# Optimization experiments

Measured on AMD Instinct MI355X. Metric: run time of the kernel, lower is better.

The kernel has to match this reference:

```python
import jax, jax.numpy as jnp
import numpy as np

B, D3, DQ, H, UNITS, SK = 32, 1024, 1024, 1024, 1024, 1024


def setup_inputs() -> dict:
    key = jax.random.key(0)
    ks = jax.random.split(key, 11)
    return {
        "K": jax.random.normal(ks[0], (B, SK, UNITS), jnp.float32),
        "Q": jax.random.normal(ks[1], (B, DQ, D3), jnp.float32),
        "M": jax.random.normal(ks[2], (B, D3, D3), jnp.float32),
        "ht": jax.random.normal(ks[3], (B, D3, H), jnp.float32),
        "Wp": jax.random.normal(ks[4], (D3, DQ), jnp.float32) * 0.02,
        "bp": jax.random.normal(ks[5], (D3,), jnp.float32) * 0.02,
        "W3": jax.random.normal(ks[6], (D3, D3), jnp.float32) * 0.02,
        "W4": jax.random.normal(ks[7], (D3, D3), jnp.float32) * 0.02,
        "b3": jax.random.normal(ks[8], (D3,), jnp.float32) * 0.02,
        "Wd": jax.random.normal(ks[9], (H + D3, UNITS), jnp.float32) * 0.02,
        "bd": jax.random.normal(ks[10], (UNITS,), jnp.float32) * 0.02,
    }


def reference(K, Q, M, ht, Wp, bp, W3, W4, b3, Wd, bd):
    # q = Wp @ Q + bp  -> (B, d3, d3); bp broadcasts over the last axis
    q = jnp.einsum('ij,bjk->bik', Wp, Q) + bp
    # concat([ht, q], axis=-1) -> (B, d3, h + d3), then fresh Dense(units)
    concat = jnp.concatenate([ht, q], axis=-1)
    mlp = jnp.einsum('bdc,cu->bdu', concat, Wd) + bd  # (B, d3, units)
    # scores = K @ mlp^T, softmax over last axis (computed but unused in the
    # original layer's output -- kept for faithfulness; DCE'd under jit)
    scores = jnp.einsum('bsu,bdu->bsd', K, mlp)       # (B, sK, d3)
    distribution = jax.nn.softmax(scores, axis=-1)
    del distribution
    # Belta = relu(W3 @ M + W4 @ q + b3), gated multiply with q
    Belta = jax.nn.relu(
        jnp.einsum('ij,bjk->bik', W3, M)
        + jnp.einsum('ij,bjk->bik', W4, q)
        + b3
    )
    q_new = Belta * q  # (B, d3, d3)
    return q_new
```

## Files before the change

### kernel.cpp

```cpp
#include <hip/hip_runtime.h>
#include <hip/hip_bf16.h>
#include <stdint.h>


#define D_ 1024

typedef __attribute__((ext_vector_type(8))) short short8;
typedef __attribute__((ext_vector_type(4))) float floatx4;
typedef __attribute__((ext_vector_type(4))) unsigned short us4;

__device__ __forceinline__ unsigned short f2bf(float f) {
  union { float f; unsigned int u; } v; v.f = f;
  unsigned int u = v.u;
  unsigned int r = (u + 0x7FFFu + ((u >> 16) & 1u)) >> 16;
  return (unsigned short)r;
}

__device__ __forceinline__ float bf2f(unsigned short h) {
  union { unsigned int u; float f; } v; v.u = ((unsigned int)h) << 16;
  return v.f;
}

__device__ __forceinline__ void async_load16(const void* g, void* l) {
  __builtin_amdgcn_global_load_lds(
      (const __attribute__((address_space(1))) unsigned int*)g,
      (__attribute__((address_space(3))) unsigned int*)l, 16, 0, 0);
}

__global__ __launch_bounds__(256) void transpose_cvt(
    const float* __restrict__ in, unsigned short* __restrict__ out) {
  __shared__ float tile[64][65];
  const int b = blockIdx.z;
  const long base = ((long)b) << 20;
  const int r0 = blockIdx.y * 64, c0 = blockIdx.x * 64;
  const int t = threadIdx.x;
  const int tr = t >> 4, tc4 = (t & 15) * 4;
#pragma unroll
  for (int p = 0; p < 4; ++p) {
    const int row = p * 16 + tr;
    const float4 v = *(const float4*)&in[base + (long)(r0 + row) * D_ + c0 + tc4];
    tile[row][tc4 + 0] = v.x; tile[row][tc4 + 1] = v.y;
    tile[row][tc4 + 2] = v.z; tile[row][tc4 + 3] = v.w;
  }
  __syncthreads();
#pragma unroll
  for (int p = 0; p < 4; ++p) {
    const int c = p * 16 + tr;
    us4 pk;
    pk.x = f2bf(tile[tc4 + 0][c]);
    pk.y = f2bf(tile[tc4 + 1][c]);
    pk.z = f2bf(tile[tc4 + 2][c]);
    pk.w = f2bf(tile[tc4 + 3][c]);
    *(us4*)&out[base + (long)(c0 + c) * D_ + r0 + tc4] = pk;
  }
}

__global__ __launch_bounds__(256) void convert_weights(
    const float* __restrict__ Wp, const float* __restrict__ W3,
    const float* __restrict__ W4, unsigned short* __restrict__ Wpb,
    unsigned short* __restrict__ A2) {
  const int i = blockIdx.x * 256 + threadIdx.x;
  const long e = (long)i * 4;
  const int row = (int)(e >> 10);
  const int col = (int)(e & 1023);
  const float4 a = ((const float4*)Wp)[i];
  us4 pa; pa.x = f2bf(a.x); pa.y = f2bf(a.y); pa.z = f2bf(a.z); pa.w = f2bf(a.w);
  ((us4*)Wpb)[i] = pa;
  const float4 w3 = ((const float4*)W3)[i];
  us4 p3; p3.x = f2bf(w3.x); p3.y = f2bf(w3.y); p3.z = f2bf(w3.z); p3.w = f2bf(w3.w);
  *(us4*)&A2[(long)row * 2048 + col] = p3;
  const float4 w4 = ((const float4*)W4)[i];
  us4 p4; p4.x = f2bf(w4.x); p4.y = f2bf(w4.y); p4.z = f2bf(w4.z); p4.w = f2bf(w4.w);
  *(us4*)&A2[(long)row * 2048 + 1024 + col] = p4;
}

__global__ __launch_bounds__(256) void gemm1(
    const unsigned short* __restrict__ Wpb,
    const unsigned short* __restrict__ Qt,
    const float* __restrict__ bp,
    unsigned short* __restrict__ qt) {
  __shared__ __align__(16) unsigned short As[128 * 64];
  __shared__ __align__(16) unsigned short Bs[128 * 64];
  const int lane = threadIdx.x & 63;
  const int wave = threadIdx.x >> 6;
  const int b = blockIdx.z;
  const int m0 = blockIdx.y * 128, n0 = blockIdx.x * 128;
  const long bb = ((long)b) << 20;
  const int wm = (wave >> 1) * 64, wn = (wave & 1) * 64;

  const int srow = wave * 32 + (lane >> 3);
  const int scol = (lane & 7) * 8;

  const unsigned short* ag = Wpb + (long)(m0 + srow) * D_ + scol;
  const unsigned short* bg = Qt + bb + (long)(n0 + srow) * D_ + scol;

  floatx4 acc[4][4] = {};

  for (int kk = 0; kk < D_; kk += 64) {
    if (kk) __syncthreads();
#pragma unroll
    for (int t = 0; t < 4; ++t) {
      async_load16(ag + (long)t * 8 * D_ + kk, &As[(wave * 32 + t * 8) * 64]);
      async_load16(bg + (long)t * 8 * D_ + kk, &Bs[(wave * 32 + t * 8) * 64]);
    }
    __syncthreads();
#pragma unroll
    for (int k2 = 0; k2 < 64; k2 += 32) {
      const int krd = k2 + (lane >> 4) * 8;
      short8 af[4], bf[4];
#pragma unroll
      for (int mt = 0; mt < 4; ++mt)
        af[mt] = *(const short8*)&As[(wm + mt * 16 + (lane & 15)) * 64 + krd];
#pragma unroll
      for (int nt = 0; nt < 4; ++nt)
        bf[nt] = *(const short8*)&Bs[(wn + nt * 16 + (lane & 15)) * 64 + krd];
#pragma unroll
      for (int mt = 0; mt < 4; ++mt)
#pragma unroll
        for (int nt = 0; nt < 4; ++nt)
          acc[mt][nt] = __builtin_amdgcn_mfma_f32_16x16x32_bf16(
              af[mt], bf[nt], acc[mt][nt], 0, 0, 0);
    }
  }

  const int quad = lane >> 4;
#pragma unroll
  for (int nt = 0; nt < 4; ++nt) {
    const int col = n0 + wn + nt * 16 + (lane & 15);
    const float bias = bp[col];
#pragma unroll
    for (int mt = 0; mt < 4; ++mt) {
      const int row = m0 + wm + mt * 16 + quad * 4;
      const floatx4 v = acc[mt][nt];
      us4 pk;
      pk.x = f2bf(v.x + bias); pk.y = f2bf(v.y + bias);
      pk.z = f2bf(v.z + bias); pk.w = f2bf(v.w + bias);
      *(us4*)&qt[bb + (long)col * D_ + row] = pk;
    }
  }
}

__global__ __launch_bounds__(256) void gemm2(
    const unsigned short* __restrict__ A2,
    const unsigned short* __restrict__ Mt,
    const unsigned short* __restrict__ qt,
    const float* __restrict__ b3,
    float* __restrict__ out) {
  __shared__ __align__(16) unsigned short As[128 * 64];
  __shared__ __align__(16) unsigned short Bs[128 * 64];
  const int lane = threadIdx.x & 63;
  const int wave = threadIdx.x >> 6;
  const int b = blockIdx.z;
  const int m0 = blockIdx.y * 128, n0 = blockIdx.x * 128;
  const long bb = ((long)b) << 20;
  const int wm = (wave >> 1) * 64, wn = (wave & 1) * 64;

  const int srow = wave * 32 + (lane >> 3);
  const int scol = (lane & 7) * 8;

  const unsigned short* ag = A2 + (long)(m0 + srow) * 2048 + scol;
  const unsigned short* bg1 = Mt + bb + (long)(n0 + srow) * D_ + scol;
  const unsigned short* bg2 = qt + bb + (long)(n0 + srow) * D_ + scol;

  floatx4 acc[4][4] = {};

  for (int kk = 0; kk < 2048; kk += 64) {
    if (kk) __syncthreads();
    const unsigned short* bg = (kk < 1024) ? (bg1 + kk) : (bg2 + (kk - 1024));
#pragma unroll
    for (int t = 0; t < 4; ++t) {
      async_load16(ag + (long)t * 8 * 2048 + kk, &As[(wave * 32 + t * 8) * 64]);
      async_load16(bg + (long)t * 8 * D_, &Bs[(wave * 32 + t * 8) * 64]);
    }
    __syncthreads();
#pragma unroll
    for (int k2 = 0; k2 < 64; k2 += 32) {
      const int krd = k2 + (lane >> 4) * 8;
      short8 af[4], bf[4];
#pragma unroll
      for (int mt = 0; mt < 4; ++mt)
        af[mt] = *(const short8*)&As[(wm + mt * 16 + (lane & 15)) * 64 + krd];
#pragma unroll
      for (int nt = 0; nt < 4; ++nt)
        bf[nt] = *(const short8*)&Bs[(wn + nt * 16 + (lane & 15)) * 64 + krd];
#pragma unroll
      for (int mt = 0; mt < 4; ++mt)
#pragma unroll
        for (int nt = 0; nt < 4; ++nt)
          acc[mt][nt] = __builtin_amdgcn_mfma_f32_16x16x32_bf16(
              af[mt], bf[nt], acc[mt][nt], 0, 0, 0);
    }
  }

  const int quad = lane >> 4;
#pragma unroll
  for (int nt = 0; nt < 4; ++nt) {
    const int col = n0 + wn + nt * 16 + (lane & 15);
    const float b3v = b3[col];
#pragma unroll
    for (int mt = 0; mt < 4; ++mt) {
      const int row = m0 + wm + mt * 16 + quad * 4;
      const floatx4 v = acc[mt][nt];
      const us4 qv = *(const us4*)&qt[bb + (long)col * D_ + row];
      float t0 = fmaxf(v.x + b3v, 0.0f);
      float t1 = fmaxf(v.y + b3v, 0.0f);
      float t2 = fmaxf(v.z + b3v, 0.0f);
      float t3 = fmaxf(v.w + b3v, 0.0f);
      out[bb + (long)(row + 0) * D_ + col] = t0 * bf2f(qv.x);
      out[bb + (long)(row + 1) * D_ + col] = t1 * bf2f(qv.y);
      out[bb + (long)(row + 2) * D_ + col] = t2 * bf2f(qv.z);
      out[bb + (long)(row + 3) * D_ + col] = t3 * bf2f(qv.w);
    }
  }
}

extern "C" void kernel_launch(void* const* d_in, const int* in_sizes, int n_in,
                              void* d_out, int out_size, void* d_ws, size_t ws_size,
                              hipStream_t stream) {
  const float* Q  = (const float*)d_in[1];
  const float* M  = (const float*)d_in[2];
  const float* Wp = (const float*)d_in[4];
  const float* bp = (const float*)d_in[5];
  const float* W3 = (const float*)d_in[6];
  const float* W4 = (const float*)d_in[7];
  const float* b3 = (const float*)d_in[8];
  float* out = (float*)d_out;

  char* ws = (char*)d_ws;
  unsigned short* qt  = (unsigned short*)(ws);
  unsigned short* Qt  = (unsigned short*)(ws + (64l  << 20));
  unsigned short* Mt  = (unsigned short*)(ws + (128l << 20));
  unsigned short* Wpb = (unsigned short*)(ws + (192l << 20));
  unsigned short* A2  = (unsigned short*)(ws + (194l << 20));

  dim3 tgrid(16, 16, 32);
  transpose_cvt<<<tgrid, 256, 0, stream>>>(Q, Qt);
  transpose_cvt<<<tgrid, 256, 0, stream>>>(M, Mt);
  convert_weights<<<1024, 256, 0, stream>>>(Wp, W3, W4, Wpb, A2);

  dim3 ggrid(8, 8, 32);
  gemm1<<<ggrid, 256, 0, stream>>>(Wpb, Qt, bp, qt);
  gemm2<<<ggrid, 256, 0, stream>>>(A2, Mt, qt, b3, out);
}
```

Baseline: 759.4 us.

## Replace GEMMs with 256x256 double-buffered 8-wave ping-pong MFMA kernel

Replaces the two 128x128 single-buffered GEMM kernels with one templated 256x256-tile kernel using 8 waves, double-buffered LDS, XOR-swizzled LDS layout, and phased MFMA blocks interleaved with async global-to-LDS loads and s_setprio. The block index is swizzled so neighbouring blocks share batches and tiles. The aim is to hide load latency behind compute, cut LDS bank conflicts and raise data reuse per tile. In exchange the kernel uses 128 KB of LDS and many accumulator registers, and it relies on explicit waitcnt and barrier placement being correct.

```diff
diff --git a/kernel.cpp b/kernel.cpp
--- a/kernel.cpp
+++ b/kernel.cpp
@@ -1,5 +1,4 @@
 #include <hip/hip_runtime.h>
-#include <hip/hip_bf16.h>
 #include <stdint.h>
 
 
@@ -8,6 +7,9 @@
 typedef __attribute__((ext_vector_type(8))) short short8;
 typedef __attribute__((ext_vector_type(4))) float floatx4;
 typedef __attribute__((ext_vector_type(4))) unsigned short us4;
+
+#define VMCNT0() asm volatile("s_waitcnt vmcnt(0)" ::: "memory")
+#define LGKM0()  asm volatile("s_waitcnt lgkmcnt(0)" ::: "memory")
 
 __device__ __forceinline__ unsigned short f2bf(float f) {
   union { float f; unsigned int u; } v; v.f = f;
@@ -74,142 +76,195 @@
   *(us4*)&A2[(long)row * 2048 + 1024 + col] = p4;
 }
 
-__global__ __launch_bounds__(256) void gemm1(
-    const unsigned short* __restrict__ Wpb,
-    const unsigned short* __restrict__ Qt,
-    const float* __restrict__ bp,
-    unsigned short* __restrict__ qt) {
-  __shared__ __align__(16) unsigned short As[128 * 64];
-  __shared__ __align__(16) unsigned short Bs[128 * 64];
+template <int NT, int LDA, bool IS_G2>
+__global__ __launch_bounds__(512, 2) void gemm8p(
+    const unsigned short* __restrict__ A,
+    const unsigned short* __restrict__ B1,
+    const unsigned short* __restrict__ B2,
+    const float* __restrict__ bias,
+    void* __restrict__ outp) {
+  __shared__ __align__(16) unsigned short As[2][256 * 64];
+  __shared__ __align__(16) unsigned short Bs[2][256 * 64];
+
   const int lane = threadIdx.x & 63;
-  const int wave = threadIdx.x >> 6;
-  const int b = blockIdx.z;
-  const int m0 = blockIdx.y * 128, n0 = blockIdx.x * 128;
+  const int w = threadIdx.x >> 6;
+  const int wm = (w >> 2) * 128;
+  const int wn = (w & 3) * 64;
+  const int l15 = lane & 15;
+  const int quad = lane >> 4;
+
+  const int bid = blockIdx.x;
+  const int swz = (bid & 7) * 64 + (bid >> 3);
+  const int b = swz >> 4;
+  const int m0 = ((swz >> 2) & 3) * 256;
+  const int n0 = (swz & 3) * 256;
   const long bb = ((long)b) << 20;
-  const int wm = (wave >> 1) * 64, wn = (wave & 1) * 64;
-
-  const int srow = wave * 32 + (lane >> 3);
-  const int scol = (lane & 7) * 8;
-
-  const unsigned short* ag = Wpb + (long)(m0 + srow) * D_ + scol;
-  const unsigned short* bg = Qt + bb + (long)(n0 + srow) * D_ + scol;
-
-  floatx4 acc[4][4] = {};
-
-  for (int kk = 0; kk < D_; kk += 64) {
-    if (kk) __syncthreads();
-#pragma unroll
-    for (int t = 0; t < 4; ++t) {
-      async_load16(ag + (long)t * 8 * D_ + kk, &As[(wave * 32 + t * 8) * 64]);
-      async_load16(bg + (long)t * 8 * D_ + kk, &Bs[(wave * 32 + t * 8) * 64]);
+
+  const int sr = lane >> 3;
+  const int sc = ((lane & 7) ^ sr) * 8;
+
+  const unsigned short* Ag = A + (long)(m0 + w * 16 + sr) * LDA + sc;
+  const unsigned short* Bg1 = B1 + bb + (long)(n0 + w * 16 + sr) * D_ + sc;
+  const unsigned short* Bg2 =
+      B2 ? (B2 + bb + (long)(n0 + w * 16 + sr) * D_ + sc) : (const unsigned short*)0;
+
+  const int kx0 = (quad * 16) ^ ((lane & 7) << 4);
+  const int kx1 = (64 + quad * 16) ^ ((lane & 7) << 4);
+
+  floatx4 acc[8][4] = {};
+
+  auto stageA = [&](int buf, int kt) {
+#pragma unroll
+    for (int h = 0; h < 2; ++h)
+#pragma unroll
+      for (int j = 0; j < 2; ++j)
+        async_load16(Ag + (long)(h * 128 + j * 8) * LDA + (long)kt * 64,
+                     &As[buf][(h * 128 + w * 16 + j * 8) * 64]);
+  };
+  auto stageB = [&](int buf, int kt) {
+    const unsigned short* bs;
+    if constexpr (IS_G2) {
+      bs = (kt < 16) ? (Bg1 + (long)kt * 64) : (Bg2 + (long)(kt - 16) * 64);
+    } else {
+      bs = Bg1 + (long)kt * 64;
     }
-    __syncthreads();
-#pragma unroll
-    for (int k2 = 0; k2 < 64; k2 += 32) {
-      const int krd = k2 + (lane >> 4) * 8;
-      short8 af[4], bf[4];
-#pragma unroll
-      for (int mt = 0; mt < 4; ++mt)
-        af[mt] = *(const short8*)&As[(wm + mt * 16 + (lane & 15)) * 64 + krd];
-#pragma unroll
-      for (int nt = 0; nt < 4; ++nt)
-        bf[nt] = *(const short8*)&Bs[(wn + nt * 16 + (lane & 15)) * 64 + krd];
-#pragma unroll
-      for (int mt = 0; mt < 4; ++mt)
-#pragma unroll
-        for (int nt = 0; nt < 4; ++nt)
-          acc[mt][nt] = __builtin_amdgcn_mfma_f32_16x16x32_bf16(
-              af[mt], bf[nt], acc[mt][nt], 0, 0, 0);
+#pragma unroll
+    for (int h = 0; h < 2; ++h)
+#pragma unroll
+      for (int j = 0; j < 2; ++j)
+        async_load16(bs + (long)(h * 128 + j * 8) * D_,
+                     &Bs[buf][(h * 128 + w * 16 + j * 8) * 64]);
+  };
+
+  auto ldA = [&](int buf, int fi, int kx) -> short8 {
+    return *(const short8*)((const char*)&As[buf][0] +
+                            (long)((wm + fi * 16 + l15) * 128 + kx));
+  };
+  auto ldB = [&](int buf, int fi, int kx) -> short8 {
+    return *(const short8*)((const char*)&Bs[buf][0] +
+                            (long)((wn + fi * 16 + l15) * 128 + kx));
+  };
+
+  stageA(0, 0);
+  stageB(0, 0);
+  VMCNT0();
+  __builtin_amdgcn_s_barrier();
+
+  short8 a[4][2], bq[2][2];
+
+  auto tile = [&](int t, int buf, bool st) {
+#pragma unroll
+    for (int r = 0; r < 4; ++r) { a[r][0] = ldA(buf, r, kx0); a[r][1] = ldA(buf, r, kx1); }
+#pragma unroll
+    for (int c = 0; c < 2; ++c) { bq[c][0] = ldB(buf, c, kx0); bq[c][1] = ldB(buf, c, kx1); }
+    if (st) stageA(buf ^ 1, t + 1);
+    __builtin_amdgcn_s_barrier();
+    LGKM0();
+    __builtin_amdgcn_sched_barrier(0);
+    __builtin_amdgcn_s_setprio(1);
+#pragma unroll
+    for (int r = 0; r < 4; ++r)
+#pragma unroll
+      for (int c = 0; c < 2; ++c)
+#pragma unroll
+        for (int ks = 0; ks < 2; ++ks)
+          acc[r][c] = __builtin_amdgcn_mfma_f32_16x16x32_bf16(
+              a[r][ks], bq[c][ks], acc[r][c], 0, 0, 0);
+    __builtin_amdgcn_s_setprio(0);
+    __builtin_amdgcn_s_barrier();
+
+#pragma unroll
+    for (int c = 0; c < 2; ++c) { bq[c][0] = ldB(buf, 2 + c, kx0); bq[c][1] = ldB(buf, 2 + c, kx1); }
+    if (st) stageB(buf ^ 1, t + 1);
+    __builtin_amdgcn_s_barrier();
+    LGKM0();
+    __builtin_amdgcn_sched_barrier(0);
+    __builtin_amdgcn_s_setprio(1);
+#pragma unroll
+    for (int r = 0; r < 4; ++r)
+#pragma unroll
+      for (int c = 0; c < 2; ++c)
+#pragma unroll
+        for (int ks = 0; ks < 2; ++ks)
+          acc[r][2 + c] = __builtin_amdgcn_mfma_f32_16x16x32_bf16(
+              a[r][ks], bq[c][ks], acc[r][2 + c], 0, 0, 0);
+    __builtin_amdgcn_s_setprio(0);
+    __builtin_amdgcn_s_barrier();
+
+#pragma unroll
+    for (int r = 0; r < 4; ++r) { a[r][0] = ldA(buf, 4 + r, kx0); a[r][1] = ldA(buf, 4 + r, kx1); }
+    __builtin_amdgcn_s_barrier();
+    LGKM0();
+    __builtin_amdgcn_sched_barrier(0);
+    __builtin_amdgcn_s_setprio(1);
+#pragma unroll
+    for (int r = 0; r < 4; ++r)
+#pragma unroll
+      for (int c = 0; c < 2; ++c)
+#pragma unroll
+        for (int ks = 0; ks < 2; ++ks)
+          acc[4 + r][2 + c] = __builtin_amdgcn_mfma_f32_16x16x32_bf16(
+              a[r][ks], bq[c][ks], acc[4 + r][2 + c], 0, 0, 0);
+    __builtin_amdgcn_s_setprio(0);
+    __builtin_amdgcn_s_barrier();
+
+#pragma unroll
+    for (int c = 0; c < 2; ++c) { bq[c][0] = ldB(buf, c, kx0); bq[c][1] = ldB(buf, c, kx1); }
+    __builtin_amdgcn_s_barrier();
+    LGKM0();
+    __builtin_amdgcn_sched_barrier(0);
+    __builtin_amdgcn_s_setprio(1);
+#pragma unroll
+    for (int r = 0; r < 4; ++r)
+#pragma unroll
+      for (int c = 0; c < 2; ++c)
+#pragma unroll
+        for (int ks = 0; ks < 2; ++ks)
+          acc[4 + r][c] = __builtin_amdgcn_mfma_f32_16x16x32_bf16(
+              a[r][ks], bq[c][ks], acc[4 + r][c], 0, 0, 0);
+    __builtin_amdgcn_s_setprio(0);
+    VMCNT0();
+    __builtin_amdgcn_s_barrier();
+  };
+
+#pragma unroll 1
+  for (int tt = 0; tt < NT; tt += 2) {
+    tile(tt, 0, true);
+    tile(tt + 1, 1, tt + 2 < NT);
+  }
+
+  if constexpr (!IS_G2) {
+    unsigned short* qt = (unsigned short*)outp;
+#pragma unroll
+    for (int c = 0; c < 4; ++c) {
+      const int col = n0 + wn + c * 16 + l15;
+      const float bv = bias[col];
+#pragma unroll
+      for (int r = 0; r < 8; ++r) {
+        const int row = m0 + wm + r * 16 + quad * 4;
+        const floatx4 v = acc[r][c];
+        us4 pk;
+        pk.x = f2bf(v.x + bv); pk.y = f2bf(v.y + bv);
+        pk.z = f2bf(v.z + bv); pk.w = f2bf(v.w + bv);
+        *(us4*)&qt[bb + (long)col * D_ + row] = pk;
+      }
     }
-  }
-
-  const int quad = lane >> 4;
-#pragma unroll
-  for (int nt = 0; nt < 4; ++nt) {
-    const int col = n0 + wn + nt * 16 + (lane & 15);
-    const float bias = bp[col];
-#pragma unroll
-    for (int mt = 0; mt < 4; ++mt) {
-      const int row = m0 + wm + mt * 16 + quad * 4;
-      const floatx4 v = acc[mt][nt];
-      us4 pk;
-      pk.x = f2bf(v.x + bias); pk.y = f2bf(v.y + bias);
-      pk.z = f2bf(v.z + bias); pk.w = f2bf(v.w + bias);
-      *(us4*)&qt[bb + (long)col * D_ + row] = pk;
-    }
-  }
-}
-
-__global__ __launch_bounds__(256) void gemm2(
-    const unsigned short* __restrict__ A2,
-    const unsigned short* __restrict__ Mt,
-    const unsigned short* __restrict__ qt,
-    const float* __restrict__ b3,
-    float* __restrict__ out) {
-  __shared__ __align__(16) unsigned short As[128 * 64];
-  __shared__ __align__(16) unsigned short Bs[128 * 64];
-  const int lane = threadIdx.x & 63;
-  const int wave = threadIdx.x >> 6;
-  const int b = blockIdx.z;
-  const int m0 = blockIdx.y * 128, n0 = blockIdx.x * 128;
-  const long bb = ((long)b) << 20;
-  const int wm = (wave >> 1) * 64, wn = (wave & 1) * 64;
-
-  const int srow = wave * 32 + (lane >> 3);
-  const int scol = (lane & 7) * 8;
-
-  const unsigned short* ag = A2 + (long)(m0 + srow) * 2048 + scol;
-  const unsigned short* bg1 = Mt + bb + (long)(n0 + srow) * D_ + scol;
-  const unsigned short* bg2 = qt + bb + (long)(n0 + srow) * D_ + scol;
-
-  floatx4 acc[4][4] = {};
-
-  for (int kk = 0; kk < 2048; kk += 64) {
-    if (kk) __syncthreads();
-    const unsigned short* bg = (kk < 1024) ? (bg1 + kk) : (bg2 + (kk - 1024));
-#pragma unroll
-    for (int t = 0; t < 4; ++t) {
-      async_load16(ag + (long)t * 8 * 2048 + kk, &As[(wave * 32 + t * 8) * 64]);
-      async_load16(bg + (long)t * 8 * D_, &Bs[(wave * 32 + t * 8) * 64]);
-    }
-    __syncthreads();
-#pragma unroll
-    for (int k2 = 0; k2 < 64; k2 += 32) {
-      const int krd = k2 + (lane >> 4) * 8;
-      short8 af[4], bf[4];
-#pragma unroll
-      for (int mt = 0; mt < 4; ++mt)
-        af[mt] = *(const short8*)&As[(wm + mt * 16 + (lane & 15)) * 64 + krd];
-#pragma unroll
-      for (int nt = 0; nt < 4; ++nt)
-        bf[nt] = *(const short8*)&Bs[(wn + nt * 16 + (lane & 15)) * 64 + krd];
-#pragma unroll
-      for (int mt = 0; mt < 4; ++mt)
-#pragma unroll
-        for (int nt = 0; nt < 4; ++nt)
-          acc[mt][nt] = __builtin_amdgcn_mfma_f32_16x16x32_bf16(
-              af[mt], bf[nt], acc[mt][nt], 0, 0, 0);
-    }
-  }
-
-  const int quad = lane >> 4;
-#pragma unroll
-  for (int nt = 0; nt < 4; ++nt) {
-    const int col = n0 + wn + nt * 16 + (lane & 15);
-    const float b3v = b3[col];
-#pragma unroll
-    for (int mt = 0; mt < 4; ++mt) {
-      const int row = m0 + wm + mt * 16 + quad * 4;
-      const floatx4 v = acc[mt][nt];
-      const us4 qv = *(const us4*)&qt[bb + (long)col * D_ + row];
-      float t0 = fmaxf(v.x + b3v, 0.0f);
-      float t1 = fmaxf(v.y + b3v, 0.0f);
-      float t2 = fmaxf(v.z + b3v, 0.0f);
-      float t3 = fmaxf(v.w + b3v, 0.0f);
-      out[bb + (long)(row + 0) * D_ + col] = t0 * bf2f(qv.x);
-      out[bb + (long)(row + 1) * D_ + col] = t1 * bf2f(qv.y);
-      out[bb + (long)(row + 2) * D_ + col] = t2 * bf2f(qv.z);
-      out[bb + (long)(row + 3) * D_ + col] = t3 * bf2f(qv.w);
+  } else {
+    float* outv = (float*)outp;
+#pragma unroll
+    for (int c = 0; c < 4; ++c) {
+      const int col = n0 + wn + c * 16 + l15;
+      const float bv = bias[col];
+#pragma unroll
+      for (int r = 0; r < 8; ++r) {
+        const int row = m0 + wm + r * 16 + quad * 4;
+        const floatx4 v = acc[r][c];
+        const us4 qv = *(const us4*)&B2[bb + (long)col * D_ + row];
+        outv[bb + (long)(row + 0) * D_ + col] = fmaxf(v.x + bv, 0.0f) * bf2f(qv.x);
+        outv[bb + (long)(row + 1) * D_ + col] = fmaxf(v.y + bv, 0.0f) * bf2f(qv.y);
+        outv[bb + (long)(row + 2) * D_ + col] = fmaxf(v.z + bv, 0.0f) * bf2f(qv.z);
+        outv[bb + (long)(row + 3) * D_ + col] = fmaxf(v.w + bv, 0.0f) * bf2f(qv.w);
+      }
     }
   }
 }
@@ -238,7 +293,8 @@
   transpose_cvt<<<tgrid, 256, 0, stream>>>(M, Mt);
   convert_weights<<<1024, 256, 0, stream>>>(Wp, W3, W4, Wpb, A2);
 
-  dim3 ggrid(8, 8, 32);
-  gemm1<<<ggrid, 256, 0, stream>>>(Wpb, Qt, bp, qt);
-  gemm2<<<ggrid, 256, 0, stream>>>(A2, Mt, qt, b3, out);
-}
+  gemm8p<16, 1024, false><<<dim3(512), dim3(512), 0, stream>>>(
+      Wpb, Qt, (const unsigned short*)nullptr, bp, qt);
+  gemm8p<32, 2048, true><<<dim3(512), dim3(512), 0, stream>>>(
+      A2, Mt, qt, b3, out);
+}
```

New measurement: 680.5 us. 10.4% less time.
